# Performance work log

Hardware: AMD Instinct MI355X
Metric: run time of the kernel (lower is better)

## Reference

```python
import jax, jax.numpy as jnp
import numpy as np

B, Cin, Cout, H, W, K = 8, 256, 256, 64, 64, 3  # kernel 3x3, stride 1, pad 1, dilation 1
EPS = 1e-5


def setup_inputs() -> dict:
    key = jax.random.key(0)
    k0, k1, k2 = jax.random.split(key, 3)
    x = jax.random.normal(k0, (B, Cin, H, W), jnp.float32)
    # offset-predicting conv (mmcv zero-inits it; use small random weights so offsets are nontrivial)
    w_off = jax.random.normal(k1, (2 * K * K, Cin, K, K), jnp.float32) * 0.01
    b_off = jnp.zeros((2 * K * K,), jnp.float32)
    # main deformable conv weight
    w = jax.random.normal(k2, (Cout, Cin, K, K), jnp.float32) * (1.0 / np.sqrt(Cin * K * K))
    b = jnp.zeros((Cout,), jnp.float32)
    gamma = jnp.ones((Cout,), jnp.float32)
    beta = jnp.zeros((Cout,), jnp.float32)
    return {"x": x, "w_off": w_off, "b_off": b_off, "w": w, "b": b, "gamma": gamma, "beta": beta}


def _deform_fusion(x, w_off, b_off, w, b, gamma, beta):
    Bn, C, Hh, Ww = x.shape
    # 1) predict offsets: [B, 2*K*K, H, W]; channel layout is (dy, dx) per kernel tap
    offset = jax.lax.conv_general_dilated(x, w_off, (1, 1), ((1, 1), (1, 1)))
    offset = offset + b_off[None, :, None, None]
    off = offset.reshape(Bn, K * K, 2, Hh, Ww)
    dy, dx = off[:, :, 0], off[:, :, 1]  # each [B, K*K, H, W]

    # 2) sampling positions: p = p0 + p_k + delta_p  (stride 1, pad 1 -> p_k in {-1,0,1})
    kk = jnp.arange(K * K)
    ky = (kk // K - (K // 2)).astype(jnp.float32)[None, :, None, None]
    kx = (kk % K - (K // 2)).astype(jnp.float32)[None, :, None, None]
    py = ky + jnp.arange(Hh, dtype=jnp.float32)[None, None, :, None] + dy  # [B,K2,H,W]
    px = kx + jnp.arange(Ww, dtype=jnp.float32)[None, None, None, :] + dx

    # 3) bilinear sampling with zero padding outside the image
    y0 = jnp.floor(py); x0 = jnp.floor(px)
    fy = py - y0; fx = px - x0
    x_flat = x.reshape(Bn, C, Hh * Ww)

    def corner(yi, xi, wgt):
        valid = (yi >= 0) & (yi <= Hh - 1) & (xi >= 0) & (xi <= Ww - 1)
        idx = (jnp.clip(yi, 0, Hh - 1) * Ww + jnp.clip(xi, 0, Ww - 1)).astype(jnp.int32)
        idx = idx.reshape(Bn, -1)  # [B, K2*H*W]
        g = jax.vmap(lambda xf, ii: jnp.take(xf, ii, axis=1))(x_flat, idx)  # [B,C,K2*H*W]
        return g * (wgt * valid).reshape(Bn, 1, -1)

    sampled = (corner(y0,     x0,     (1 - fy) * (1 - fx))
             + corner(y0,     x0 + 1, (1 - fy) * fx)
             + corner(y0 + 1, x0,     fy * (1 - fx))
             + corner(y0 + 1, x0 + 1, fy * fx))  # [B, C, K2*H*W]
    sampled = sampled.reshape(Bn, C, K * K, Hh * Ww)

    # 4) contract sampled patches with conv weight: implicit-GEMM of deformable conv
    out = jnp.einsum('bckp,ock->bop', sampled, w.reshape(w.shape[0], C, K * K))
    out = out + b[None, :, None]
    out = out.reshape(Bn, -1, Hh, Ww)

    # 5) BatchNorm (training-mode batch statistics) + ReLU
    mean = out.mean(axis=(0, 2, 3), keepdims=True)
    var = out.var(axis=(0, 2, 3), keepdims=True)
    out = gamma[None, :, None, None] * (out - mean) * jax.lax.rsqrt(var + EPS) + beta[None, :, None, None]
    return jax.nn.relu(out)


def reference(x, w_off, b_off, w, b, gamma, beta):
    return _deform_fusion(x, w_off, b_off, w, b, gamma, beta)
```

## Files before the change

### kernel.cpp

```cpp
#include <hip/hip_runtime.h>
#include <math.h>

#define BN_ 8
#define CIN 256
#define COUT 256
#define HH 64
#define WW 64
#define HW 4096
#define KK 9
#define OC 18
#define EPS 1e-5f
#define NTOT (BN_ * COUT * HW)

#define WTB_WS 589824
#define WOB_WS 884736
#define ST_WS  921600
#define XT_WS  922112

typedef float f32x4 __attribute__((ext_vector_type(4)));
typedef float f32x2 __attribute__((ext_vector_type(2)));
typedef short s16x8 __attribute__((ext_vector_type(8)));
typedef unsigned int u32x4 __attribute__((ext_vector_type(4)));

__device__ __forceinline__ unsigned short f2bf(float f) {
  unsigned int u = __float_as_uint(f);
  unsigned int r = (u + 0x7fffu + ((u >> 16) & 1u)) >> 16;
  return (unsigned short)r;
}
__device__ __forceinline__ float bf2f(short s) {
  return __uint_as_float(((unsigned int)(unsigned short)s) << 16);
}

__global__ __launch_bounds__(256) void xpose_kernel(
    const float* __restrict__ x, unsigned short* __restrict__ xt) {
  __shared__ float s[64][65];
  const int t = threadIdx.x;
  const int p0 = blockIdx.x * 64;
  const int c0 = blockIdx.y * 64;
  const int b  = blockIdx.z;
  const float* xb = x + ((size_t)b * CIN + c0) * HW + p0;
#pragma unroll
  for (int pass = 0; pass < 4; ++pass) {
    int cr = pass * 16 + (t >> 4);
    int ps = (t & 15) * 4;
    float4 v = *(const float4*)(xb + (size_t)cr * HW + ps);
    s[ps + 0][cr] = v.x; s[ps + 1][cr] = v.y; s[ps + 2][cr] = v.z; s[ps + 3][cr] = v.w;
  }
  __syncthreads();
  unsigned short* xo = xt + (size_t)b * 32 * HW * 8;
#pragma unroll
  for (int r = 0; r < 2; ++r) {
    int flat = r * 256 + t;
    int pr = flat >> 3, sub = flat & 7;
    int g8 = (c0 >> 3) + sub;
    s16x8 v;
#pragma unroll
    for (int j = 0; j < 8; ++j) v[j] = (short)f2bf(s[pr][sub * 8 + j]);
    *(s16x8*)(xo + ((size_t)g8 * HW + p0 + pr) * 8) = v;
  }
}

__global__ __launch_bounds__(256) void prep_kernel(
    const float* __restrict__ w_off, const float* __restrict__ w,
    unsigned short* __restrict__ wob, unsigned short* __restrict__ wTb,
    float* __restrict__ stats) {
  const int kb = blockIdx.x;
  const int kk = kb >> 3;
  const int c0 = (kb & 7) << 5;
  const int t = threadIdx.x;
  if (kb == 71) { stats[t] = 0.f; stats[256 + t] = 0.f; }
#pragma unroll
  for (int r = 0; r < 4; ++r) {
    int e = r * 256 + t;
    int g = e >> 8, m = (e >> 3) & 31, j = e & 7;
    int c = c0 + g * 8 + j;
    unsigned short v = 0;
    if (m < OC) v = f2bf(w_off[((size_t)m * CIN + c) * 9 + kk]);
    wob[(size_t)kb * 1024 + e] = v;
  }
#pragma unroll
  for (int g = 0; g < 4; ++g)
#pragma unroll
    for (int j = 0; j < 8; ++j) {
      int c = c0 + g * 8 + j;
      wTb[(((size_t)kb * 4 + g) * 256 + t) * 8 + j] =
          f2bf(w[((size_t)t * CIN + c) * 9 + kk]);
    }
}

__global__ __launch_bounds__(1024, 4) void gemm_kernel(
    const unsigned short* __restrict__ xt, const unsigned short* __restrict__ wTb,
    const unsigned short* __restrict__ wob, const float* __restrict__ b_off,
    const float* __restrict__ bias, float* __restrict__ out,
    float* __restrict__ stats) {
  __shared__ __align__(16) char lds[81920];
  const int t = threadIdx.x;
  const int lane = t & 63;
  const int wv = t >> 6;
  const int b = blockIdx.x & 7;
  const int hh2 = blockIdx.x >> 3;
  const int p0 = hh2 * 128;
  const int col = t & 127;
  const int oct = t >> 7;
  const int fr = lane & 15, fq = lane >> 4;
  const unsigned short* xtb = xt + (size_t)b * 32 * HW * 8;
  float* s_off = (float*)(lds + 65536);
  unsigned short (*s_b)[8192] = (unsigned short(*)[8192])lds;

  {
    const int wg = wv & 7;
    const int half = wv >> 3;
    const int yrow = 2 * hh2 + half;
    unsigned short* sb = (unsigned short*)lds + wv * 2048;
    f32x4 acc_o[2][4] = {};

    auto fetch = [&](int s, s16x8* V, s16x8* AF) {
      const int ki = wg * 9 + s;
      const int kk = ki >> 3, cc0g = (ki & 7) << 2;
      const int ky = kk / 3 - 1, kx = kk % 3 - 1;
      const int y = yrow + ky;
      const int xcol = lane + kx;
      const bool ok = (y >= 0) && (y < HH) && (xcol >= 0) && (xcol < WW);
      const int pix = y * WW + xcol;
#pragma unroll
      for (int g = 0; g < 4; ++g) {
        s16x8 v = {0, 0, 0, 0, 0, 0, 0, 0};
        if (ok)
          __builtin_memcpy(&v, (const char*)xtb + (((size_t)(cc0g + g)) << 16) + (size_t)pix * 16, 16);
        V[g] = v;
      }
      const unsigned short* ap = wob + (size_t)ki * 1024;
#pragma unroll
      for (int i = 0; i < 2; ++i)
        AF[i] = *(const s16x8*)&ap[(fq * 32 + i * 16 + fr) * 8];
    };

    s16x8 VE[4], VO[4], afE2[2], afO2[2];
    fetch(0, VE, afE2);

#define OBODY(S, VC, VN, AFC, AFN)                                             \
    {                                                                          \
      _Pragma("unroll")                                                        \
      for (int g = 0; g < 4; ++g)                                              \
        *(s16x8*)&sb[(g * 64 + lane) * 8] = VC[g];                             \
      if ((S) + 1 < 9) fetch((S) + 1, VN, AFN);                                \
      s16x8 bf[4];                                                             \
      _Pragma("unroll")                                                        \
      for (int jn = 0; jn < 4; ++jn)                                           \
        bf[jn] = *(const s16x8*)&sb[(fq * 64 + jn * 16 + fr) * 8];             \
      _Pragma("unroll")                                                        \
      for (int i = 0; i < 2; ++i)                                              \
        _Pragma("unroll")                                                      \
        for (int jn = 0; jn < 4; ++jn)                                         \
          acc_o[i][jn] = __builtin_amdgcn_mfma_f32_16x16x32_bf16(              \
              AFC[i], bf[jn], acc_o[i][jn], 0, 0, 0);                          \
    }

    for (int sp = 0; sp < 4; ++sp) {
      OBODY(2 * sp, VE, VO, afE2, afO2)
      OBODY(2 * sp + 1, VO, VE, afO2, afE2)
    }
    OBODY(8, VE, VO, afE2, afO2)
#undef OBODY

    __syncthreads();
    float* red = (float*)lds;
#pragma unroll
    for (int pass = 0; pass < 2; ++pass) {
      if (half == pass) {
#pragma unroll
        for (int i = 0; i < 2; ++i)
#pragma unroll
          for (int jn = 0; jn < 4; ++jn)
#pragma unroll
            for (int rg = 0; rg < 4; ++rg)
              red[wg * 2048 + (i * 16 + fq * 4 + rg) * 64 + jn * 16 + fr] = acc_o[i][jn][rg];
      }
      __syncthreads();
      {
        const int f2 = t * 2;
        const int m = f2 >> 6;
        f32x2 v = {0.f, 0.f};
#pragma unroll
        for (int w = 0; w < 8; ++w) {
          f32x2 a = *(f32x2*)&red[w * 2048 + f2];
          v[0] += a[0]; v[1] += a[1];
        }
        float bo = (m < OC) ? b_off[m] : 0.f;
        v[0] += bo; v[1] += bo;
        *(f32x2*)&s_off[m * 128 + pass * 64 + (f2 & 63)] = v;
      }
      __syncthreads();
    }
  }

  int cofs[4];
  f32x2 qw2[4];

  auto calc = [&](int kk) {
    float dy = s_off[(2 * kk) * 128 + col];
    float dx = s_off[(2 * kk + 1) * 128 + col];
    int y = 2 * hh2 + (col >> 6);
    int xx = col & 63;
    float py = (float)(kk / 3 - 1 + y) + dy;
    float pxx = (float)(kk % 3 - 1 + xx) + dx;
    float y0f = floorf(py), x0f = floorf(pxx);
    float fy = py - y0f, fx = pxx - x0f;
    int y0 = (int)y0f, x0 = (int)x0f;
    int y1 = y0 + 1, x1 = x0 + 1;
    bool vy0 = (y0 >= 0) && (y0 < HH), vy1 = (y1 >= 0) && (y1 < HH);
    bool vx0 = (x0 >= 0) && (x0 < WW), vx1 = (x1 >= 0) && (x1 < WW);
    int cy0 = min(max(y0, 0), HH - 1), cy1 = min(max(y1, 0), HH - 1);
    int cx0 = min(max(x0, 0), WW - 1), cx1 = min(max(x1, 0), WW - 1);
    float q0 = (vy0 && vx0) ? (1.f - fy) * (1.f - fx) : 0.f;
    float q1 = (vy0 && vx1) ? (1.f - fy) * fx : 0.f;
    float q2 = (vy1 && vx0) ? fy * (1.f - fx) : 0.f;
    float q3 = (vy1 && vx1) ? fy * fx : 0.f;
    cofs[0] = (cy0 * WW + cx0) * 16;  qw2[0][0] = q0; qw2[0][1] = q0;
    cofs[1] = (cy0 * WW + cx1) * 16;  qw2[1][0] = q1; qw2[1][1] = q1;
    cofs[2] = (cy1 * WW + cx0) * 16;  qw2[2][0] = q2; qw2[2][1] = q2;
    cofs[3] = (cy1 * WW + cx1) * 16;  qw2[3][0] = q3; qw2[3][1] = q3;
  };

  s16x8 g[4];

  auto gather = [&](int chunk64) {
    const char* bp = (const char*)xtb + (((size_t)(chunk64 * 8 + oct)) << 16);
#pragma unroll
    for (int k = 0; k < 4; ++k)
      __builtin_memcpy(&g[k], bp + cofs[k], 16);
  };

  auto combine_write = [&](int buf) {
    u32x4 vout;
#pragma unroll
    for (int jp = 0; jp < 4; ++jp) {
      f32x2 a = {0.f, 0.f};
#pragma unroll
      for (int k = 0; k < 4; ++k) {
        unsigned int pr = ((const unsigned int*)&g[k])[jp];
        f32x2 xv;
        xv[0] = __uint_as_float(pr << 16);
        xv[1] = __uint_as_float(pr & 0xffff0000u);
        a = __builtin_elementwise_fma(qw2[k], xv, a);
      }
      unsigned int packed;
      asm("v_cvt_pk_bf16_f32 %0, %1, %2" : "=v"(packed) : "v"(a[0]), "v"(a[1]));
      vout[jp] = packed;
    }
    *(u32x4*)&s_b[buf][(oct * 128 + col) * 8] = vout;
  };

  auto load_a = [&](int iter, s16x8 af[2]) {
#pragma unroll
    for (int ks = 0; ks < 2; ++ks)
      af[ks] = *(const s16x8*)&wTb[(((size_t)(iter * 2 + ks) * 4 + fq) * 256 + wv * 16 + fr) * 8];
  };

  f32x4 acc[8] = {};
  s16x8 afE[2], afO[2];

  {
    calc(0);
    gather(0);
    load_a(0, afE);
    combine_write(0);
  }
  asm volatile("s_waitcnt lgkmcnt(0)" ::: "memory");
  __builtin_amdgcn_s_barrier();

#define GBODY(I, AFC, AFN, CUR)                                                \
  {                                                                            \
    const int nx1 = (I) + 1;                                                   \
    if (nx1 < 36) {                                                            \
      if ((nx1 & 3) == 0) calc(nx1 >> 2);                                      \
      gather(nx1 & 3);                                                         \
      load_a(nx1, AFN);                                                        \
    }                                                                          \
    __builtin_amdgcn_s_setprio(1);                                             \
    _Pragma("unroll")                                                          \
    for (int ks = 0; ks < 2; ++ks)                                             \
      _Pragma("unroll")                                                        \
      for (int jj = 0; jj < 8; ++jj) {                                         \
        s16x8 bfr = *(const s16x8*)&s_b[CUR][((ks * 4 + fq) * 128 + jj * 16 + fr) * 8]; \
        acc[jj] = __builtin_amdgcn_mfma_f32_16x16x32_bf16(                     \
            AFC[ks], bfr, acc[jj], 0, 0, 0);                                   \
      }                                                                        \
    __builtin_amdgcn_s_setprio(0);                                             \
    if (nx1 < 36) {                                                            \
      combine_write((CUR) ^ 1);                                                \
      asm volatile("s_waitcnt lgkmcnt(0)" ::: "memory");                       \
      __builtin_amdgcn_s_barrier();                                            \
    }                                                                          \
  }

  for (int m = 0; m < 18; ++m) {
    const int i0 = 2 * m;
    GBODY(i0, afE, afO, 0)
    GBODY(i0 + 1, afO, afE, 1)
  }
#undef GBODY

#pragma unroll
  for (int rg = 0; rg < 4; ++rg) {
    int o = wv * 16 + fq * 4 + rg;
    float bv = bias[o];
    float* op = out + ((size_t)(b * COUT + o)) * HW + p0 + fr;
    float s = 0.f, s2 = 0.f;
#pragma unroll
    for (int j = 0; j < 8; ++j) {
      float val = acc[j][rg] + bv;
      op[j * 16] = val;
      s += val; s2 += val * val;
    }
#pragma unroll
    for (int m2 = 1; m2 < 16; m2 <<= 1) {
      s += __shfl_xor(s, m2);
      s2 += __shfl_xor(s2, m2);
    }
    if (fr == 0) {
      atomicAdd(&stats[o], s);
      atomicAdd(&stats[COUT + o], s2);
    }
  }
}

__global__ __launch_bounds__(256) void bn_kernel(
    float* __restrict__ out, const float* __restrict__ stats,
    const float* __restrict__ gamma, const float* __restrict__ beta) {
  int i4 = (blockIdx.x * 256 + threadIdx.x) * 4;
  int o = (i4 >> 12) & (COUT - 1);
  const float inv_n = 1.f / (float)(BN_ * HW);
  float mean = stats[o] * inv_n;
  float var = stats[COUT + o] * inv_n - mean * mean;
  float sc = gamma[o] * rsqrtf(var + EPS);
  float sh = beta[o] - mean * sc;
  float4 v = *(float4*)(out + i4);
  v.x = fmaxf(fmaf(v.x, sc, sh), 0.f);
  v.y = fmaxf(fmaf(v.y, sc, sh), 0.f);
  v.z = fmaxf(fmaf(v.z, sc, sh), 0.f);
  v.w = fmaxf(fmaf(v.w, sc, sh), 0.f);
  *(float4*)(out + i4) = v;
}

extern "C" void kernel_launch(void* const* d_in, const int* in_sizes, int n_in,
                              void* d_out, int out_size, void* d_ws, size_t ws_size,
                              hipStream_t stream) {
  const float* x     = (const float*)d_in[0];
  const float* w_off = (const float*)d_in[1];
  const float* b_off = (const float*)d_in[2];
  const float* w     = (const float*)d_in[3];
  const float* bias  = (const float*)d_in[4];
  const float* gamma = (const float*)d_in[5];
  const float* beta  = (const float*)d_in[6];
  float* out = (float*)d_out;
  float* ws = (float*)d_ws;
  unsigned short* wTb = (unsigned short*)(ws + WTB_WS);
  unsigned short* wob = (unsigned short*)(ws + WOB_WS);
  float* stats = ws + ST_WS;
  unsigned short* xt = (unsigned short*)(ws + XT_WS);

  xpose_kernel<<<dim3(64, 4, 8), 256, 0, stream>>>(x, xt);
  prep_kernel<<<72, 256, 0, stream>>>(w_off, w, wob, wTb, stats);
  gemm_kernel<<<256, 1024, 0, stream>>>(xt, wTb, wob, b_off, bias, out, stats);
  bn_kernel<<<NTOT / 1024, 256, 0, stream>>>(out, stats, gamma, beta);
}
```

Baseline: 200.8 us.

## Prefetch bilinear corner gathers two iterations ahead with double-buffered registers

The global gathers of the four bilinear corners are issued two main-loop iterations ahead and held in alternating register sets (gE/gO), so their latency is hidden behind a full MFMA step instead of one. Corner addresses are kept as pointers that advance by one channel chunk per gather, and the interpolation weights for the next tap are staged in a separate set and swapped in after the combine. This raises register pressure and now runs the barrier on every iteration, including the last one.

After: 234.0 us. 16.5% more time.

```diff
diff --git a/kernel.cpp b/kernel.cpp
--- a/kernel.cpp
+++ b/kernel.cpp
@@ -194,10 +194,10 @@
     }
   }
 
-  int cofs[4];
-  f32x2 qw2[4];
-
-  auto calc = [&](int kk) {
+  f32x2 qw2[4], qwN[4];
+  const char* ga[4];
+
+  auto calc = [&](int kk, int chunk64) {
     float dy = s_off[(2 * kk) * 128 + col];
     float dx = s_off[(2 * kk + 1) * 128 + col];
     int y = 2 * hh2 + (col >> 6);
@@ -216,22 +216,24 @@
     float q1 = (vy0 && vx1) ? (1.f - fy) * fx : 0.f;
     float q2 = (vy1 && vx0) ? fy * (1.f - fx) : 0.f;
     float q3 = (vy1 && vx1) ? fy * fx : 0.f;
-    cofs[0] = (cy0 * WW + cx0) * 16;  qw2[0][0] = q0; qw2[0][1] = q0;
-    cofs[1] = (cy0 * WW + cx1) * 16;  qw2[1][0] = q1; qw2[1][1] = q1;
-    cofs[2] = (cy1 * WW + cx0) * 16;  qw2[2][0] = q2; qw2[2][1] = q2;
-    cofs[3] = (cy1 * WW + cx1) * 16;  qw2[3][0] = q3; qw2[3][1] = q3;
+    const char* bp = (const char*)xtb + (((size_t)(chunk64 * 8 + oct)) << 16);
+    ga[0] = bp + (cy0 * WW + cx0) * 16;  qwN[0][0] = q0; qwN[0][1] = q0;
+    ga[1] = bp + (cy0 * WW + cx1) * 16;  qwN[1][0] = q1; qwN[1][1] = q1;
+    ga[2] = bp + (cy1 * WW + cx0) * 16;  qwN[2][0] = q2; qwN[2][1] = q2;
+    ga[3] = bp + (cy1 * WW + cx1) * 16;  qwN[3][0] = q3; qwN[3][1] = q3;
   };
 
-  s16x8 g[4];
-
-  auto gather = [&](int chunk64) {
-    const char* bp = (const char*)xtb + (((size_t)(chunk64 * 8 + oct)) << 16);
-#pragma unroll
-    for (int k = 0; k < 4; ++k)
-      __builtin_memcpy(&g[k], bp + cofs[k], 16);
+  s16x8 gE[4], gO[4];
+
+  auto gather = [&](s16x8* g) {
+#pragma unroll
+    for (int k = 0; k < 4; ++k) {
+      __builtin_memcpy(&g[k], ga[k], 16);
+      ga[k] += 8 << 16;
+    }
   };
 
-  auto combine_write = [&](int buf) {
+  auto combine_write = [&](int buf, const s16x8* g) {
     u32x4 vout;
 #pragma unroll
     for (int jp = 0; jp < 4; ++jp) {
@@ -261,20 +263,26 @@
   s16x8 afE[2], afO[2];
 
   {
-    calc(0);
-    gather(0);
+    calc(0, 0);
+#pragma unroll
+    for (int k2 = 0; k2 < 4; ++k2) qw2[k2] = qwN[k2];
+    gather(gE);
     load_a(0, afE);
-    combine_write(0);
+    combine_write(0, gE);
+    gather(gO);
   }
   asm volatile("s_waitcnt lgkmcnt(0)" ::: "memory");
   __builtin_amdgcn_s_barrier();
 
-#define GBODY(I, AFC, AFN, CUR)                                                \
+#define GBODY(I, AFC, AFN, GW, GR, CUR)                                        \
   {                                                                            \
-    const int nx1 = (I) + 1;                                                   \
+    const int nx1 = (I) + 1, nx2 = (I) + 2;                                    \
+    bool newq = false;                                                         \
     if (nx1 < 36) {                                                            \
-      if ((nx1 & 3) == 0) calc(nx1 >> 2);                                      \
-      gather(nx1 & 3);                                                         \
+      if (nx2 < 36) {                                                          \
+        if ((nx2 & 3) == 0) { calc(nx2 >> 2, 0); newq = true; }                \
+        gather(GW);                                                            \
+      }                                                                        \
       load_a(nx1, AFN);                                                        \
     }                                                                          \
     __builtin_amdgcn_s_setprio(1);                                             \
@@ -288,16 +296,20 @@
       }                                                                        \
     __builtin_amdgcn_s_setprio(0);                                             \
     if (nx1 < 36) {                                                            \
-      combine_write((CUR) ^ 1);                                                \
-      asm volatile("s_waitcnt lgkmcnt(0)" ::: "memory");                       \
-      __builtin_amdgcn_s_barrier();                                            \
+      combine_write((CUR) ^ 1, GR);                                            \
+      if (newq) {                                                              \
+        _Pragma("unroll")                                                      \
+        for (int k2 = 0; k2 < 4; ++k2) qw2[k2] = qwN[k2];                      \
+      }                                                                        \
     }                                                                          \
+    asm volatile("s_waitcnt lgkmcnt(0)" ::: "memory");                         \
+    __builtin_amdgcn_s_barrier();                                              \
   }
 
   for (int m = 0; m < 18; ++m) {
     const int i0 = 2 * m;
-    GBODY(i0, afE, afO, 0)
-    GBODY(i0 + 1, afO, afE, 1)
+    GBODY(i0, afE, afO, gE, gO, 0)
+    GBODY(i0 + 1, afO, afE, gO, gE, 1)
   }
 #undef GBODY
 
```
